# Kernel optimization log

Measured on AMD Instinct MI355X. Metric: run time of the kernel, lower is better.

The kernel has to match this reference:

```python
import jax, jax.numpy as jnp
import numpy as np

DIM_HEAD = 64
HEADS = 8

def rotate_half(x):
    x1, x2 = jnp.split(x, 2, axis=-1)
    return jnp.concatenate((-x2, x1), axis=-1)

def apply_rope(pos, t):
    # pos: [N, d] broadcast against t: [B, H, N, d]
    return t * jnp.cos(pos) + rotate_half(t) * jnp.sin(pos)

def setup_inputs() -> dict:
    key = jax.random.key(0)
    k1, k2, k3, k4 = jax.random.split(key, 4)
    B, N, C = 2, 4096, 512
    inner = HEADS * DIM_HEAD
    x = jax.random.normal(k1, (B, N, C), dtype=jnp.float32)
    pos_emb = jax.random.normal(k2, (N, DIM_HEAD), dtype=jnp.float32)
    w_qkv = jax.random.normal(k3, (C, inner * 3), dtype=jnp.float32) * (1.0 / np.sqrt(C))
    w_out = jax.random.normal(k4, (inner, C), dtype=jnp.float32) * (1.0 / np.sqrt(inner))
    b_out = jnp.zeros((C,), dtype=jnp.float32)
    return {"x": x, "pos_emb": pos_emb, "w_qkv": w_qkv, "w_out": w_out, "b_out": b_out}

def reference(x, pos_emb, w_qkv, w_out, b_out):
    B, N, C = x.shape
    scale = DIM_HEAD ** -0.5
    qkv = x @ w_qkv  # [B, N, 3*inner]
    q, k, v = jnp.split(qkv, 3, axis=-1)
    def to_heads(t):
        return t.reshape(B, N, HEADS, DIM_HEAD).transpose(0, 2, 1, 3)  # [B,H,N,d]
    q, k, v = to_heads(q), to_heads(k), to_heads(v)
    q = apply_rope(pos_emb, q)
    k = apply_rope(pos_emb, k)
    dots = jnp.einsum('bhid,bhjd->bhij', q, k) * scale  # [B,H,N,N]
    attn = jax.nn.softmax(dots, axis=-1)
    out = jnp.einsum('bhij,bhjd->bhid', attn, v)
    out = out.transpose(0, 2, 1, 3).reshape(B, N, HEADS * DIM_HEAD)
    return out @ w_out + b_out
```

## Files before the change

kernel.cpp:

```cpp
#include <hip/hip_runtime.h>


typedef float    floatx4 __attribute__((ext_vector_type(4)));
typedef _Float16 half8   __attribute__((ext_vector_type(8)));
typedef _Float16 half4   __attribute__((ext_vector_type(4)));
typedef unsigned uintx4  __attribute__((ext_vector_type(4)));

__device__ __forceinline__ float fast_exp2(float x) {
#if __has_builtin(__builtin_amdgcn_exp2f)
  return __builtin_amdgcn_exp2f(x);
#else
  float r;
  asm("v_exp_f32 %0, %1" : "=v"(r) : "v"(x));
  return r;
#endif
}

__device__ __forceinline__ void async16(const void* g, void* l) {
  __builtin_amdgcn_global_load_lds(
      (const __attribute__((address_space(1))) void*)g,
      (__attribute__((address_space(3))) void*)l, 16, 0, 0);
}

__device__ __forceinline__ void pl32swap(unsigned& a, unsigned& b) {
  asm("v_permlane32_swap_b32 %0, %1" : "+v"(a), "+v"(b));
}

__global__ __launch_bounds__(256) void prep(
    const float* __restrict__ X, const float* __restrict__ pos,
    const float* __restrict__ Wqkv, const float* __restrict__ Wout,
    _Float16* __restrict__ A2, float2* __restrict__ CSSN,
    _Float16* __restrict__ B2qkv, _Float16* __restrict__ B2out) {
  __shared__ float tile[64][65];
  const int bid = blockIdx.x, t = threadIdx.x;
  if (bid < 4096) {
    const int i = (bid * 256 + t) * 4;
    const float4 v = *(const float4*)(X + i);
    half4 h;
    h[0] = (_Float16)v.x; h[1] = (_Float16)v.y;
    h[2] = (_Float16)v.z; h[3] = (_Float16)v.w;
    *(half4*)(A2 + i) = h;
  } else if (bid < 5120) {
    const int i = (bid - 4096) * 256 + t;
    const float p = pos[i];
    CSSN[i] = make_float2(__cosf(p), __sinf(p));
  } else {
    const float* W; _Float16* B2T; int Ncols, bx, by;
    if (bid < 5312) { const int idx = bid - 5120; bx = idx % 24; by = idx / 24;
                      W = Wqkv; B2T = B2qkv; Ncols = 1536; }
    else            { const int idx = bid - 5312; bx = idx % 8;  by = idx / 8;
                      W = Wout; B2T = B2out; Ncols = 512; }
    const int k0 = by * 64, n0 = bx * 64;
    const int lane = t & 63, w = t >> 6;
#pragma unroll 4
    for (int i = 0; i < 16; ++i) {
      const int k = w * 16 + i;
      tile[k][lane] = W[(size_t)(k0 + k) * Ncols + n0 + lane];
    }
    __syncthreads();
#pragma unroll 4
    for (int i = 0; i < 16; ++i) {
      const int n = w * 16 + i;
      B2T[(size_t)(n0 + n) * 512 + k0 + lane] = (_Float16)tile[lane][n];
    }
  }
}

__global__ __launch_bounds__(256) void gemm_qkv_rope(
    const _Float16* __restrict__ A2, const _Float16* __restrict__ B2T,
    const float2* __restrict__ CSSN,
    _Float16* __restrict__ Qb, _Float16* __restrict__ Kb,
    _Float16* __restrict__ VT) {
  __shared__ __align__(16) _Float16 ldsA[128 * 64];
  __shared__ __align__(16) _Float16 ldsB[128 * 64];
  __shared__ __align__(16) _Float16 qk_lds[4][16][72];
  const int t = threadIdx.x, w = t >> 6, l = t & 63;
  const int lo = l & 15, hi = l >> 4, sw = lo & 7;
  const int m0 = blockIdx.y << 7, n0 = blockIdx.x << 7;

  const int strow = w * 8 + (l >> 3);
  const int schunk = (l & 7) ^ ((l >> 3) & 7);
  const _Float16* gA = A2 + (size_t)(m0 + strow) * 512 + schunk * 8;
  const _Float16* gB = B2T + (size_t)(n0 + strow) * 512 + schunk * 8;
  _Float16* lA = ldsA + w * 512 + l * 8;
  _Float16* lB = ldsB + w * 512 + l * 8;

  const int mw = (w >> 1) * 64, nw = (w & 1) * 64;

  floatx4 acc[4][4];
#pragma unroll
  for (int mt = 0; mt < 4; ++mt)
#pragma unroll
    for (int nt = 0; nt < 4; ++nt) acc[mt][nt] = (floatx4){0.f, 0.f, 0.f, 0.f};

  for (int ks = 0; ks < 8; ++ks) {
    const int kk = ks * 64;
    __syncthreads();
#pragma unroll
    for (int i = 0; i < 4; ++i) {
      async16(gA + (size_t)i * 32 * 512 + kk, lA + i * 2048);
      async16(gB + (size_t)i * 32 * 512 + kk, lB + i * 2048);
    }
    __syncthreads();
#pragma unroll
    for (int kc = 0; kc < 2; ++kc) {
      const int slot = ((hi + 4 * kc) ^ sw) * 8;
      half8 af[4], bf[4];
#pragma unroll
      for (int mt = 0; mt < 4; ++mt)
        af[mt] = *(const half8*)(ldsA + (mw + mt * 16 + lo) * 64 + slot);
#pragma unroll
      for (int nt = 0; nt < 4; ++nt)
        bf[nt] = *(const half8*)(ldsB + (nw + nt * 16 + lo) * 64 + slot);
#pragma unroll
      for (int mt = 0; mt < 4; ++mt)
#pragma unroll
        for (int nt = 0; nt < 4; ++nt)
          acc[mt][nt] = __builtin_amdgcn_mfma_f32_16x16x32_f16(
              af[mt], bf[nt], acc[mt][nt], 0, 0, 0);
    }
  }

  const int bx = blockIdx.x;
  const int kind = bx >> 2;
  const int h = ((bx & 3) << 1) | (nw >> 6);
  if (kind == 2) {
#pragma unroll
    for (int mt = 0; mt < 4; ++mt) {
      const int rowb = m0 + mw + mt * 16 + hi * 4;
      const int b = rowb >> 12, nn = rowb & 4095;
#pragma unroll
      for (int nt = 0; nt < 4; ++nt) {
        const int dd = nt * 16 + lo;
        half4 v4;
#pragma unroll
        for (int r = 0; r < 4; ++r) v4[r] = (_Float16)acc[mt][nt][r];
        *(half4*)(VT + ((size_t)((b * 8 + h) * 64 + dd)) * 4096 + nn) = v4;
      }
    }
  } else {
    _Float16* Db = (kind == 0) ? Qb : Kb;
    const float sc = (kind == 0) ? 0.125f * 1.44269504f : 1.0f;
    _Float16 (*qt_)[72] = qk_lds[w];
#pragma unroll
    for (int mt = 0; mt < 4; ++mt) {
#pragma unroll
      for (int r = 0; r < 4; ++r) {
        const int row = m0 + mw + mt * 16 + hi * 4 + r;
        const int nn = row & 4095;
        const float2* cp = CSSN + (size_t)nn * 64 + lo;
#pragma unroll
        for (int nt = 0; nt < 4; ++nt) {
          const float2 cs = cp[nt * 16];
          const float x0 = acc[mt][nt][r];
          const float xp = acc[mt][nt ^ 2][r];
          const float rot = (nt & 2) ? xp : -xp;
          qt_[hi * 4 + r][nt * 16 + lo] = (_Float16)((x0 * cs.x + rot * cs.y) * sc);
        }
      }
#pragma unroll
      for (int pass = 0; pass < 2; ++pass) {
        const int rr = pass * 8 + (l >> 3);
        const int dcol = (l & 7) * 8;
        const half8 v = *(const half8*)&qt_[rr][dcol];
        const int row = m0 + mw + mt * 16 + rr;
        const int b = row >> 12, nn = row & 4095;
        *(half8*)(Db + ((size_t)((b * 8 + h) * 4096 + nn)) * 64 + dcol) = v;
      }
    }
  }
}

__global__ __launch_bounds__(256) void gemm_out_f16(
    const _Float16* __restrict__ A2, const _Float16* __restrict__ B2T,
    const float* __restrict__ bias, float* __restrict__ C) {
  __shared__ __align__(16) _Float16 ldsA[128 * 64];
  __shared__ __align__(16) _Float16 ldsB[64 * 64];
  const int t = threadIdx.x, w = t >> 6, l = t & 63;
  const int lo = l & 15, hi = l >> 4, sw = lo & 7;
  const int m0 = blockIdx.y << 7, n0 = blockIdx.x << 6;

  const int strow = w * 8 + (l >> 3);
  const int schunk = (l & 7) ^ ((l >> 3) & 7);
  const _Float16* gA = A2 + (size_t)(m0 + strow) * 512 + schunk * 8;
  const _Float16* gB = B2T + (size_t)(n0 + strow) * 512 + schunk * 8;
  _Float16* lA = ldsA + w * 512 + l * 8;
  _Float16* lB = ldsB + w * 512 + l * 8;

  const int mw = (w >> 1) * 64, nw = (w & 1) * 32;

  floatx4 acc[4][2];
#pragma unroll
  for (int mt = 0; mt < 4; ++mt)
#pragma unroll
    for (int nt = 0; nt < 2; ++nt) acc[mt][nt] = (floatx4){0.f, 0.f, 0.f, 0.f};

  for (int ks = 0; ks < 8; ++ks) {
    const int kk = ks * 64;
    __syncthreads();
#pragma unroll
    for (int i = 0; i < 4; ++i)
      async16(gA + (size_t)i * 32 * 512 + kk, lA + i * 2048);
#pragma unroll
    for (int i = 0; i < 2; ++i)
      async16(gB + (size_t)i * 32 * 512 + kk, lB + i * 2048);
    __syncthreads();
#pragma unroll
    for (int kc = 0; kc < 2; ++kc) {
      const int slot = ((hi + 4 * kc) ^ sw) * 8;
      half8 af[4], bf[2];
#pragma unroll
      for (int mt = 0; mt < 4; ++mt)
        af[mt] = *(const half8*)(ldsA + (mw + mt * 16 + lo) * 64 + slot);
#pragma unroll
      for (int nt = 0; nt < 2; ++nt)
        bf[nt] = *(const half8*)(ldsB + (nw + nt * 16 + lo) * 64 + slot);
#pragma unroll
      for (int mt = 0; mt < 4; ++mt)
#pragma unroll
        for (int nt = 0; nt < 2; ++nt)
          acc[mt][nt] = __builtin_amdgcn_mfma_f32_16x16x32_f16(
              af[mt], bf[nt], acc[mt][nt], 0, 0, 0);
    }
  }
#pragma unroll
  for (int mt = 0; mt < 4; ++mt)
#pragma unroll
    for (int r = 0; r < 4; ++r) {
      const int row = m0 + mw + mt * 16 + hi * 4 + r;
#pragma unroll
      for (int nt = 0; nt < 2; ++nt) {
        const int col = n0 + nw + nt * 16 + lo;
        C[(size_t)row * 512 + col] = acc[mt][nt][r] + bias[col];
      }
    }
}

__global__ __launch_bounds__(256, 4) void flash_attn(
    const _Float16* __restrict__ Qb, const _Float16* __restrict__ Kb,
    const _Float16* __restrict__ VT, _Float16* __restrict__ Opart,
    float* __restrict__ lpart) {
  __shared__ __align__(16) _Float16 ldsK[2][64 * 64];
  __shared__ __align__(16) _Float16 ldsV[2][64 * 64];
  const int t = threadIdx.x;
  const int w = t >> 6, l = t & 63;
  const int lo = l & 15, hi = l >> 4;
  const int sw = lo & 7;
  const int lop = (lo & 3) | ((lo & 4) << 1) | ((lo & 8) >> 1);
  const int swk = lop & 7;
  const int bh = blockIdx.y, qt = blockIdx.x, sp = blockIdx.z;

  const int srow = l >> 3;
  const int scol = (l & 7) ^ srow;
  const int goffK = srow * 64 + scol * 8;
  const size_t goffV = (size_t)srow * 4096 + scol * 8;
  const int ldst = l * 8;

  const _Float16* Qrow = Qb + ((size_t)bh * 4096 + qt * 128 + w * 32 + lo) * 64;
  half8 qf[2][2];
  qf[0][0] = *(const half8*)(Qrow + hi * 8);
  qf[0][1] = *(const half8*)(Qrow + hi * 8 + 32);
  qf[1][0] = *(const half8*)(Qrow + 16 * 64 + hi * 8);
  qf[1][1] = *(const half8*)(Qrow + 16 * 64 + hi * 8 + 32);

  floatx4 acc[2][4];
  float l_s[2] = {0.f, 0.f};
#pragma unroll
  for (int g = 0; g < 2; ++g)
#pragma unroll
    for (int dt = 0; dt < 4; ++dt) acc[g][dt] = (floatx4){0.f, 0.f, 0.f, 0.f};

  const _Float16* Kt = Kb + (size_t)bh * 4096 * 64;
  const _Float16* Vt = VT + (size_t)bh * 64 * 4096;

  auto stage = [&](int buf, int tt) {
    const _Float16* gK = Kt + (size_t)tt * 4096;
    const _Float16* gV = Vt + tt * 64;
    _Float16* dK = &ldsK[buf][0];
    _Float16* dV = &ldsV[buf][0];
    const int k0 = w * 2;
    async16(gK + (size_t)k0 * 512 + goffK,         dK + k0 * 512 + ldst);
    async16(gK + (size_t)(k0 + 1) * 512 + goffK,   dK + (k0 + 1) * 512 + ldst);
    async16(gV + (size_t)k0 * 32768 + goffV,       dV + k0 * 512 + ldst);
    async16(gV + (size_t)(k0 + 1) * 32768 + goffV, dV + (k0 + 1) * 512 + ldst);
  };

  stage(0, sp * 32);
  for (int it = 0; it < 32; ++it) {
    const int cur = it & 1;
    __syncthreads();
    if (it != 31) stage(cur ^ 1, sp * 32 + it + 1);
    const _Float16* ldsKc = &ldsK[cur][0];
    const _Float16* ldsVc = &ldsV[cur][0];

    floatx4 st[2][4];
    __builtin_amdgcn_s_setprio(1);
#pragma unroll
    for (int jt = 0; jt < 4; ++jt) {
      const _Float16* kr = ldsKc + (jt * 16 + lop) * 64;
      const half8 kf0 = *(const half8*)(kr + ((hi ^ swk) * 8));
      const half8 kf1 = *(const half8*)(kr + (((hi + 4) ^ swk) * 8));
#pragma unroll
      for (int g = 0; g < 2; ++g) {
        floatx4 z = (floatx4){0.f, 0.f, 0.f, 0.f};
        z = __builtin_amdgcn_mfma_f32_16x16x32_f16(kf0, qf[g][0], z, 0, 0, 0);
        z = __builtin_amdgcn_mfma_f32_16x16x32_f16(kf1, qf[g][1], z, 0, 0, 0);
        st[g][jt] = z;
      }
    }
    __builtin_amdgcn_s_setprio(0);

    half8 paf0[2];
#pragma unroll
    for (int g = 0; g < 2; ++g) {
      const float a0 = fast_exp2(st[g][0][0]);
      const float a1 = fast_exp2(st[g][0][1]);
      const float a2 = fast_exp2(st[g][0][2]);
      const float a3 = fast_exp2(st[g][0][3]);
      l_s[g] += (a0 + a1) + (a2 + a3);
      unsigned x0 = __builtin_bit_cast(unsigned, __builtin_amdgcn_cvt_pkrtz(a0, a1));
      unsigned y0 = __builtin_bit_cast(unsigned, __builtin_amdgcn_cvt_pkrtz(a2, a3));
      const float b0 = fast_exp2(st[g][1][0]);
      const float b1 = fast_exp2(st[g][1][1]);
      const float b2 = fast_exp2(st[g][1][2]);
      const float b3 = fast_exp2(st[g][1][3]);
      l_s[g] += (b0 + b1) + (b2 + b3);
      unsigned x1 = __builtin_bit_cast(unsigned, __builtin_amdgcn_cvt_pkrtz(b0, b1));
      unsigned y1 = __builtin_bit_cast(unsigned, __builtin_amdgcn_cvt_pkrtz(b2, b3));
      pl32swap(x0, x1);
      pl32swap(y0, y1);
      uintx4 u;
      u[0] = x0; u[1] = y0; u[2] = x1; u[3] = y1;
      paf0[g] = __builtin_bit_cast(half8, u);
    }
    __builtin_amdgcn_s_setprio(1);
#pragma unroll
    for (int dt = 0; dt < 4; ++dt) {
      const _Float16* vrow = ldsVc + (dt * 16 + lo) * 64;
      const half8 vf0 = *(const half8*)(vrow + ((hi ^ sw) * 8));
#pragma unroll
      for (int g = 0; g < 2; ++g)
        acc[g][dt] = __builtin_amdgcn_mfma_f32_16x16x32_f16(
            paf0[g], vf0, acc[g][dt], 0, 0, 0);
    }
    __builtin_amdgcn_s_setprio(0);

    half8 paf1[2];
#pragma unroll
    for (int g = 0; g < 2; ++g) {
      const float a0 = fast_exp2(st[g][2][0]);
      const float a1 = fast_exp2(st[g][2][1]);
      const float a2 = fast_exp2(st[g][2][2]);
      const float a3 = fast_exp2(st[g][2][3]);
      l_s[g] += (a0 + a1) + (a2 + a3);
      unsigned x0 = __builtin_bit_cast(unsigned, __builtin_amdgcn_cvt_pkrtz(a0, a1));
      unsigned y0 = __builtin_bit_cast(unsigned, __builtin_amdgcn_cvt_pkrtz(a2, a3));
      const float b0 = fast_exp2(st[g][3][0]);
      const float b1 = fast_exp2(st[g][3][1]);
      const float b2 = fast_exp2(st[g][3][2]);
      const float b3 = fast_exp2(st[g][3][3]);
      l_s[g] += (b0 + b1) + (b2 + b3);
      unsigned x1 = __builtin_bit_cast(unsigned, __builtin_amdgcn_cvt_pkrtz(b0, b1));
      unsigned y1 = __builtin_bit_cast(unsigned, __builtin_amdgcn_cvt_pkrtz(b2, b3));
      pl32swap(x0, x1);
      pl32swap(y0, y1);
      uintx4 u;
      u[0] = x0; u[1] = y0; u[2] = x1; u[3] = y1;
      paf1[g] = __builtin_bit_cast(half8, u);
    }
    __builtin_amdgcn_s_setprio(1);
#pragma unroll
    for (int dt = 0; dt < 4; ++dt) {
      const _Float16* vrow = ldsVc + (dt * 16 + lo) * 64;
      const half8 vf1 = *(const half8*)(vrow + (((4 + hi) ^ sw) * 8));
#pragma unroll
      for (int g = 0; g < 2; ++g)
        acc[g][dt] = __builtin_amdgcn_mfma_f32_16x16x32_f16(
            paf1[g], vf1, acc[g][dt], 0, 0, 0);
    }
    __builtin_amdgcn_s_setprio(0);
  }

  _Float16* obase = Opart + ((size_t)(sp * 16 + bh)) * 4096 * 64;
  float*    lbase = lpart + ((size_t)(sp * 16 + bh)) * 4096;
#pragma unroll
  for (int g = 0; g < 2; ++g) {
    float v = l_s[g];
    v += __shfl_xor(v, 16);
    v += __shfl_xor(v, 32);
    if (hi == 0)
      lbase[qt * 128 + w * 32 + g * 16 + lo] = v;
#pragma unroll
    for (int r = 0; r < 4; ++r) {
      const int q = qt * 128 + w * 32 + g * 16 + hi * 4 + r;
#pragma unroll
      for (int dt = 0; dt < 4; ++dt)
        obase[(size_t)q * 64 + dt * 16 + lo] = (_Float16)acc[g][dt][r];
    }
  }
}

__global__ __launch_bounds__(256) void combine_splits(
    const _Float16* __restrict__ Opart, const float* __restrict__ lpart,
    _Float16* __restrict__ O2) {
  const int idx = blockIdx.x * 256 + threadIdx.x;
  const int d0 = (idx & 15) * 4;
  const int q  = (idx >> 4) & 4095;
  const int bh = idx >> 16;
  const int b = bh >> 3, h = bh & 7;
  const half4 a0 = *(const half4*)(Opart + ((size_t)bh * 4096 + q) * 64 + d0);
  const half4 a1 = *(const half4*)(Opart + ((size_t)(16 + bh) * 4096 + q) * 64 + d0);
  const float lsum = lpart[(size_t)bh * 4096 + q] +
                     lpart[(size_t)(16 + bh) * 4096 + q];
  const float inv = 1.f / lsum;
  half4 o;
#pragma unroll
  for (int i = 0; i < 4; ++i)
    o[i] = (_Float16)(((float)a0[i] + (float)a1[i]) * inv);
  *(half4*)(O2 + ((size_t)(b * 4096 + q)) * 512 + h * 64 + d0) = o;
}

extern "C" void kernel_launch(void* const* d_in, const int* in_sizes, int n_in,
                              void* d_out, int out_size, void* d_ws, size_t ws_size,
                              hipStream_t stream) {
  const float* x     = (const float*)d_in[0];
  const float* pos   = (const float*)d_in[1];
  const float* w_qkv = (const float*)d_in[2];
  const float* w_out = (const float*)d_in[3];
  const float* b_out = (const float*)d_in[4];
  float* out = (float*)d_out;

  char* ws = (char*)d_ws;
  if (ws_size < (size_t)56 * 1024 * 1024) return;

  const size_t MB = 1024 * 1024;
  _Float16* A2x   = (_Float16*)ws;
  _Float16* O2    = (_Float16*)ws;
  _Float16* B2qkv = (_Float16*)(ws + 8 * MB);
  float2*   CSSN  = (float2*)(ws + 11 * MB);
  _Float16* Qb    = (_Float16*)(ws + 13 * MB);
  _Float16* Kb    = (_Float16*)(ws + 21 * MB);
  _Float16* VT    = (_Float16*)(ws + 29 * MB);
  _Float16* Opart = (_Float16*)(ws + 37 * MB);
  float*    lpart = (float*)(ws + 53 * MB);
  _Float16* B2out = (_Float16*)(ws + 54 * MB);

  prep<<<5376, 256, 0, stream>>>(x, pos, w_qkv, w_out, A2x, CSSN, B2qkv, B2out);
  gemm_qkv_rope<<<dim3(12, 64), 256, 0, stream>>>(A2x, B2qkv, CSSN, Qb, Kb, VT);
  flash_attn<<<dim3(32, 16, 2), 256, 0, stream>>>(Qb, Kb, VT, Opart, lpart);
  combine_splits<<<4096, 256, 0, stream>>>(Opart, lpart, O2);
  gemm_out_f16<<<dim3(8, 64), 256, 0, stream>>>(O2, B2out, b_out, out);
}
```

Before: 204.3 us.

## Fuse split-attention combine into output projection GEMM A-tile load

Removes the separate combine_splits kernel and its O2 intermediate buffer. The output GEMM now reads both partial attention outputs and their row sums directly, normalizes them in registers, and writes the f16 A tile into LDS with synchronous stores instead of async global-to-LDS loads. This saves one launch and one full write/read round trip of the combined activation. In exchange, each of the 8 column blocks recomputes the combine and reads twice as much A data, and the A loads are no longer asynchronous.

```diff
diff --git a/kernel.cpp b/kernel.cpp
--- a/kernel.cpp
+++ b/kernel.cpp
@@ -172,7 +172,8 @@
 }
 
 __global__ __launch_bounds__(256) void gemm_out_f16(
-    const _Float16* __restrict__ A2, const _Float16* __restrict__ B2T,
+    const _Float16* __restrict__ Opart, const float* __restrict__ lpart,
+    const _Float16* __restrict__ B2T,
     const float* __restrict__ bias, float* __restrict__ C) {
   __shared__ __align__(16) _Float16 ldsA[128 * 64];
   __shared__ __align__(16) _Float16 ldsB[64 * 64];
@@ -182,7 +183,6 @@
 
   const int strow = w * 8 + (l >> 3);
   const int schunk = (l & 7) ^ ((l >> 3) & 7);
-  const _Float16* gA = A2 + (size_t)(m0 + strow) * 512 + schunk * 8;
   const _Float16* gB = B2T + (size_t)(n0 + strow) * 512 + schunk * 8;
   _Float16* lA = ldsA + w * 512 + l * 8;
   _Float16* lB = ldsB + w * 512 + l * 8;
@@ -198,12 +198,31 @@
   for (int ks = 0; ks < 8; ++ks) {
     const int kk = ks * 64;
     __syncthreads();
-#pragma unroll
-    for (int i = 0; i < 4; ++i)
-      async16(gA + (size_t)i * 32 * 512 + kk, lA + i * 2048);
+    half8 a0[4], a1[4];
+    float inv[4];
+#pragma unroll
+    for (int i = 0; i < 4; ++i) {
+      const int row = m0 + strow + i * 32;
+      const int b = row >> 12, q = row & 4095;
+      const int k = kk + schunk * 8;
+      const int bh = b * 8 + (k >> 6);
+      const int d0 = k & 63;
+      a0[i] = *(const half8*)(Opart + ((size_t)bh * 4096 + q) * 64 + d0);
+      a1[i] = *(const half8*)(Opart + ((size_t)(16 + bh) * 4096 + q) * 64 + d0);
+      inv[i] = 1.f / (lpart[(size_t)bh * 4096 + q] +
+                      lpart[(size_t)(16 + bh) * 4096 + q]);
+    }
 #pragma unroll
     for (int i = 0; i < 2; ++i)
       async16(gB + (size_t)i * 32 * 512 + kk, lB + i * 2048);
+#pragma unroll
+    for (int i = 0; i < 4; ++i) {
+      half8 hv;
+#pragma unroll
+      for (int j = 0; j < 8; ++j)
+        hv[j] = (_Float16)(((float)a0[i][j] + (float)a1[i][j]) * inv[i]);
+      *(half8*)(lA + i * 2048) = hv;
+    }
     __syncthreads();
 #pragma unroll
     for (int kc = 0; kc < 2; ++kc) {
@@ -400,26 +419,6 @@
   }
 }
 
-__global__ __launch_bounds__(256) void combine_splits(
-    const _Float16* __restrict__ Opart, const float* __restrict__ lpart,
-    _Float16* __restrict__ O2) {
-  const int idx = blockIdx.x * 256 + threadIdx.x;
-  const int d0 = (idx & 15) * 4;
-  const int q  = (idx >> 4) & 4095;
-  const int bh = idx >> 16;
-  const int b = bh >> 3, h = bh & 7;
-  const half4 a0 = *(const half4*)(Opart + ((size_t)bh * 4096 + q) * 64 + d0);
-  const half4 a1 = *(const half4*)(Opart + ((size_t)(16 + bh) * 4096 + q) * 64 + d0);
-  const float lsum = lpart[(size_t)bh * 4096 + q] +
-                     lpart[(size_t)(16 + bh) * 4096 + q];
-  const float inv = 1.f / lsum;
-  half4 o;
-#pragma unroll
-  for (int i = 0; i < 4; ++i)
-    o[i] = (_Float16)(((float)a0[i] + (float)a1[i]) * inv);
-  *(half4*)(O2 + ((size_t)(b * 4096 + q)) * 512 + h * 64 + d0) = o;
-}
-
 extern "C" void kernel_launch(void* const* d_in, const int* in_sizes, int n_in,
                               void* d_out, int out_size, void* d_ws, size_t ws_size,
                               hipStream_t stream) {
@@ -435,7 +434,6 @@
 
   const size_t MB = 1024 * 1024;
   _Float16* A2x   = (_Float16*)ws;
-  _Float16* O2    = (_Float16*)ws;
   _Float16* B2qkv = (_Float16*)(ws + 8 * MB);
   float2*   CSSN  = (float2*)(ws + 11 * MB);
   _Float16* Qb    = (_Float16*)(ws + 13 * MB);
@@ -448,6 +446,5 @@
   prep<<<5376, 256, 0, stream>>>(x, pos, w_qkv, w_out, A2x, CSSN, B2qkv, B2out);
   gemm_qkv_rope<<<dim3(12, 64), 256, 0, stream>>>(A2x, B2qkv, CSSN, Qb, Kb, VT);
   flash_attn<<<dim3(32, 16, 2), 256, 0, stream>>>(Qb, Kb, VT, Opart, lpart);
-  combine_splits<<<4096, 256, 0, stream>>>(Opart, lpart, O2);
-  gemm_out_f16<<<dim3(8, 64), 256, 0, stream>>>(O2, B2out, b_out, out);
-}
+  gemm_out_f16<<<dim3(8, 64), 256, 0, stream>>>(Opart, lpart, B2out, b_out, out);
+}
```

Result: slower. 216.0 us (+5.8%).
